# Kernel tuning notes

Measured on AMD Instinct MI355X. Metric: run time of the kernel, lower is better.

Reference implementation:

```python
import jax, jax.numpy as jnp
import numpy as np

B, T, D = 2, 2048, 2048
Q_HEADS, KV_HEADS, HEAD_DIM = 16, 4, 128
ROPE_BASE = 10000.0


def _apply_rotary(x_nhd, positions_n):
    # x_nhd: (N, H, head_dim); half-split rotary embedding.
    half = x_nhd.shape[-1] // 2
    inv_freq = 1.0 / (ROPE_BASE ** (jnp.arange(half, dtype=jnp.float32) / half))
    ang = positions_n.astype(jnp.float32)[:, None] * inv_freq  # (N, half)
    cos = jnp.cos(ang)[:, None, :]  # (N, 1, half)
    sin = jnp.sin(ang)[:, None, :]
    x1, x2 = x_nhd[..., :half], x_nhd[..., half:]
    return jnp.concatenate([x1 * cos - x2 * sin, x1 * sin + x2 * cos], axis=-1)


def setup_inputs() -> dict:
    key = jax.random.key(0)
    ks = jax.random.split(key, 5)
    s_in = 1.0 / np.sqrt(D)
    s_o = 1.0 / np.sqrt(Q_HEADS * HEAD_DIM)
    x = jax.random.normal(ks[0], (B, T, D), dtype=jnp.float32)
    positions = jnp.broadcast_to(jnp.arange(T, dtype=jnp.int32), (B, T))
    wq = jax.random.normal(ks[1], (Q_HEADS * HEAD_DIM, D), dtype=jnp.float32) * s_in
    wk = jax.random.normal(ks[2], (KV_HEADS * HEAD_DIM, D), dtype=jnp.float32) * s_in
    wv = jax.random.normal(ks[3], (KV_HEADS * HEAD_DIM, D), dtype=jnp.float32) * s_in
    wo = jax.random.normal(ks[4], (D, Q_HEADS * HEAD_DIM), dtype=jnp.float32) * s_o
    return {"x": x, "positions": positions, "wq": wq, "wk": wk, "wv": wv, "wo": wo}


def reference(x, positions, wq, wk, wv, wo):
    bsz, tsz, _ = x.shape
    q = jnp.einsum('btd,od->bto', x, wq).reshape(bsz, tsz, Q_HEADS, HEAD_DIM)
    k = jnp.einsum('btd,od->bto', x, wk).reshape(bsz, tsz, KV_HEADS, HEAD_DIM)
    v = jnp.einsum('btd,od->bto', x, wv).reshape(bsz, tsz, KV_HEADS, HEAD_DIM)
    pos_flat = positions.reshape(-1)
    q = _apply_rotary(q.reshape(-1, Q_HEADS, HEAD_DIM), pos_flat).reshape(bsz, tsz, Q_HEADS, HEAD_DIM)
    k = _apply_rotary(k.reshape(-1, KV_HEADS, HEAD_DIM), pos_flat).reshape(bsz, tsz, KV_HEADS, HEAD_DIM)
    rep = Q_HEADS // KV_HEADS
    k = jnp.repeat(k, rep, axis=2)
    v = jnp.repeat(v, rep, axis=2)
    logits = jnp.einsum('bthd,bThd->bhtT', q, k) / jnp.sqrt(jnp.float32(HEAD_DIM))
    causal = jnp.tril(jnp.ones((tsz, tsz), dtype=bool))
    logits = jnp.where(causal[None, None], logits, -1e9)
    weights = jax.nn.softmax(logits, axis=-1)
    ctx = jnp.einsum('bhtT,bThd->bthd', weights, v).reshape(bsz, tsz, Q_HEADS * HEAD_DIM)
    return jnp.einsum('bto,do->btd', ctx, wo)
```

## Files before the change

kernel.cpp:

```cpp
#include <hip/hip_runtime.h>
#include <hip/hip_bf16.h>

typedef __bf16 bf16x8 __attribute__((ext_vector_type(8)));
typedef float  f32x4  __attribute__((ext_vector_type(4)));
typedef float  f32x16 __attribute__((ext_vector_type(16)));
typedef unsigned int u32x2 __attribute__((ext_vector_type(2)));

#define B_   2
#define T_   2048
#define D_   2048
#define QH_  16
#define KVH_ 4
#define HD_  128
#define BT_  (B_ * T_)
#define KVD_ 512
#define SCL  0.12751744f

#define GLOAD_LDS16(g, l)                                        \
  __builtin_amdgcn_global_load_lds(                              \
      (const __attribute__((address_space(1))) void*)(g),        \
      (__attribute__((address_space(3))) void*)(l), 16, 0, 0)

__global__ __launch_bounds__(256) void cvt_all(
    const float* __restrict__ x, const float* __restrict__ wq,
    const float* __restrict__ wk, const float* __restrict__ wv,
    const float* __restrict__ wo, ushort* __restrict__ out) {
  const int i = blockIdx.x * 256 + threadIdx.x;
  int j = i;
  const float* src;
  float mul = 1.f;
  if (j < 2097152) { src = x; }
  else if ((j -= 2097152) < 1048576) { src = wq; mul = SCL; }
  else if ((j -= 1048576) < 262144)  { src = wk; }
  else if ((j -= 262144) < 262144)   { src = wv; }
  else { j -= 262144; src = wo; }
  float4 v = ((const float4*)src)[j];
  __hip_bfloat16 h0 = __float2bfloat16(v.x * mul);
  __hip_bfloat16 h1 = __float2bfloat16(v.y * mul);
  __hip_bfloat16 h2 = __float2bfloat16(v.z * mul);
  __hip_bfloat16 h3 = __float2bfloat16(v.w * mul);
  ushort4 o;
  o.x = *(ushort*)&h0; o.y = *(ushort*)&h1;
  o.z = *(ushort*)&h2; o.w = *(ushort*)&h3;
  ((ushort4*)out)[i] = o;
}

__global__ __launch_bounds__(256) void gemm_qkv(
    const ushort* __restrict__ X, const ushort* __restrict__ WQ,
    const ushort* __restrict__ WK, const ushort* __restrict__ WV,
    ushort* __restrict__ qo, ushort* __restrict__ ko, ushort* __restrict__ vo) {
  const int nb = blockIdx.x % 24;
  const int mb = blockIdx.x / 24;
  const int tid = threadIdx.x;
  const int wave = tid >> 6;
  const int lane = tid & 63;
  const int mrow = lane & 15;
  const int quad = lane >> 4;
  const int wm = wave >> 1;
  const int wn = wave & 1;
  const int m0 = mb * 128;
  const int K = D_;

  const ushort* Wg;
  if (nb < 16)      Wg = WQ + (size_t)nb * 128 * K;
  else if (nb < 20) Wg = WK + (size_t)(nb - 16) * 128 * K;
  else              Wg = WV + (size_t)(nb - 20) * 128 * K;

  __shared__ __align__(16) ushort At[2][128 * 64];
  __shared__ __align__(16) ushort Bt[2][128 * 64];

  f32x4 acc[4][4];
#pragma unroll
  for (int i = 0; i < 4; ++i)
#pragma unroll
    for (int j = 0; j < 4; ++j) acc[i][j] = (f32x4){0.f, 0.f, 0.f, 0.f};

  const ushort* Xg = X + (size_t)m0 * K;

  auto STAGE = [&](int buf, int k0) {
#pragma unroll
    for (int p = 0; p < 4; ++p) {
      const int c = p * 256 + tid;
      const int row = c >> 3;
      const int cc = (c & 7) ^ (row & 7);
      GLOAD_LDS16(Xg + (size_t)row * K + k0 + cc * 8,
                  At[buf] + (size_t)(p * 256 + wave * 64) * 8);
      GLOAD_LDS16(Wg + (size_t)row * K + k0 + cc * 8,
                  Bt[buf] + (size_t)(p * 256 + wave * 64) * 8);
    }
  };

  const int NT = K / 64;
  STAGE(0, 0);
  STAGE(1, 64);

  for (int t = 0; t < NT; ++t) {
    const int cur = t & 1;
    if (t + 2 < NT) asm volatile("s_waitcnt vmcnt(8)" ::: "memory");
    else            asm volatile("s_waitcnt vmcnt(0)" ::: "memory");
    __builtin_amdgcn_s_barrier();

    const ushort* Ac = At[cur];
    const ushort* Bc = Bt[cur];
#pragma unroll
    for (int s = 0; s < 2; ++s) {
      bf16x8 af[4], bfr[4];
#pragma unroll
      for (int mt = 0; mt < 4; ++mt) {
        const int row = wm * 64 + mt * 16 + mrow;
        af[mt] = *reinterpret_cast<const bf16x8*>(
            Ac + row * 64 + (((s * 4 + quad) ^ (row & 7)) * 8));
      }
#pragma unroll
      for (int nt = 0; nt < 4; ++nt) {
        const int row = wn * 64 + nt * 16 + mrow;
        bfr[nt] = *reinterpret_cast<const bf16x8*>(
            Bc + row * 64 + (((s * 4 + quad) ^ (row & 7)) * 8));
      }
#pragma unroll
      for (int mt = 0; mt < 4; ++mt)
#pragma unroll
        for (int nt = 0; nt < 4; ++nt)
          acc[mt][nt] = __builtin_amdgcn_mfma_f32_16x16x32_bf16(
              af[mt], bfr[nt], acc[mt][nt], 0, 0, 0);
    }

    asm volatile("s_waitcnt lgkmcnt(0)" ::: "memory");
    __builtin_amdgcn_s_barrier();
    if (t + 2 < NT) STAGE(cur, (t + 2) * 64);
  }

#pragma unroll
  for (int mt = 0; mt < 4; ++mt) {
#pragma unroll
    for (int nt = 0; nt < 4; ++nt) {
      const int colw = wn * 64 + nt * 16 + mrow;
      const int row0 = m0 + wm * 64 + mt * 16 + quad * 4;
      if (nb < 16) {
        const int col = nb * 128 + colw;
#pragma unroll
        for (int r = 0; r < 4; ++r) {
          __hip_bfloat16 hh = __float2bfloat16(acc[mt][nt][r]);
          qo[(size_t)(row0 + r) * 2048 + col] = *(ushort*)&hh;
        }
      } else if (nb < 20) {
        const int col = (nb - 16) * 128 + colw;
#pragma unroll
        for (int r = 0; r < 4; ++r) {
          __hip_bfloat16 hh = __float2bfloat16(acc[mt][nt][r]);
          ko[(size_t)(row0 + r) * KVD_ + col] = *(ushort*)&hh;
        }
      } else {
        const int col = (nb - 20) * 128 + colw;
        const int bb = row0 >> 11;
        const int t0 = row0 & (T_ - 1);
        ushort4 s4;
#pragma unroll
        for (int r = 0; r < 4; ++r) {
          __hip_bfloat16 hh = __float2bfloat16(acc[mt][nt][r]);
          (&s4.x)[r] = *(ushort*)&hh;
        }
        *(ushort4*)(vo + ((size_t)(bb * KVD_ + col)) * T_ + t0) = s4;
      }
    }
  }
}

__global__ __launch_bounds__(256) void gemm_o(
    const ushort* __restrict__ X, const ushort* __restrict__ W,
    float* __restrict__ Y, int M, int N, int K) {
  const int nb128 = N >> 7;
  const int mb = blockIdx.x / nb128;
  const int nb = blockIdx.x % nb128;
  const int tid = threadIdx.x;
  const int wave = tid >> 6;
  const int lane = tid & 63;
  const int mrow = lane & 15;
  const int quad = lane >> 4;
  const int wm = wave >> 1;
  const int wn = wave & 1;
  const int m0 = mb * 128;
  const int n0 = nb * 128;

  __shared__ __align__(16) ushort At[2][128 * 64];
  __shared__ __align__(16) ushort Bt[2][128 * 64];

  f32x4 acc[4][4];
#pragma unroll
  for (int i = 0; i < 4; ++i)
#pragma unroll
    for (int j = 0; j < 4; ++j) acc[i][j] = (f32x4){0.f, 0.f, 0.f, 0.f};

  const ushort* Xg = X + (size_t)m0 * K;
  const ushort* Wg = W + (size_t)n0 * K;

  auto STAGE = [&](int buf, int k0) {
#pragma unroll
    for (int p = 0; p < 4; ++p) {
      const int c = p * 256 + tid;
      const int row = c >> 3;
      const int cc = (c & 7) ^ (row & 7);
      GLOAD_LDS16(Xg + (size_t)row * K + k0 + cc * 8,
                  At[buf] + (size_t)(p * 256 + wave * 64) * 8);
      GLOAD_LDS16(Wg + (size_t)row * K + k0 + cc * 8,
                  Bt[buf] + (size_t)(p * 256 + wave * 64) * 8);
    }
  };

  const int NT = K / 64;
  STAGE(0, 0);
  STAGE(1, 64);

  for (int t = 0; t < NT; ++t) {
    const int cur = t & 1;
    if (t + 2 < NT) asm volatile("s_waitcnt vmcnt(8)" ::: "memory");
    else            asm volatile("s_waitcnt vmcnt(0)" ::: "memory");
    __builtin_amdgcn_s_barrier();

    const ushort* Ac = At[cur];
    const ushort* Bc = Bt[cur];
#pragma unroll
    for (int s = 0; s < 2; ++s) {
      bf16x8 af[4], bfr[4];
#pragma unroll
      for (int mt = 0; mt < 4; ++mt) {
        const int row = wm * 64 + mt * 16 + mrow;
        af[mt] = *reinterpret_cast<const bf16x8*>(
            Ac + row * 64 + (((s * 4 + quad) ^ (row & 7)) * 8));
      }
#pragma unroll
      for (int nt = 0; nt < 4; ++nt) {
        const int row = wn * 64 + nt * 16 + mrow;
        bfr[nt] = *reinterpret_cast<const bf16x8*>(
            Bc + row * 64 + (((s * 4 + quad) ^ (row & 7)) * 8));
      }
#pragma unroll
      for (int mt = 0; mt < 4; ++mt)
#pragma unroll
        for (int nt = 0; nt < 4; ++nt)
          acc[mt][nt] = __builtin_amdgcn_mfma_f32_16x16x32_bf16(
              af[mt], bfr[nt], acc[mt][nt], 0, 0, 0);
    }

    asm volatile("s_waitcnt lgkmcnt(0)" ::: "memory");
    __builtin_amdgcn_s_barrier();
    if (t + 2 < NT) STAGE(cur, (t + 2) * 64);
  }

#pragma unroll
  for (int mt = 0; mt < 4; ++mt)
#pragma unroll
    for (int nt = 0; nt < 4; ++nt) {
      const int col = n0 + wn * 64 + nt * 16 + mrow;
      const int row0 = m0 + wm * 64 + mt * 16 + quad * 4;
#pragma unroll
      for (int r = 0; r < 4; ++r)
        Y[(size_t)(row0 + r) * N + col] = acc[mt][nt][r];
    }
}

__global__ __launch_bounds__(256) void rope_kernel(
    __hip_bfloat16* __restrict__ q, __hip_bfloat16* __restrict__ k,
    const int* __restrict__ positions) {
  const int wave = threadIdx.x >> 6;
  const int lane = threadIdx.x & 63;
  const int p = blockIdx.x * 4 + wave;
  const int head = p % (QH_ + KVH_);
  const int bt = p / (QH_ + KVH_);

  __hip_bfloat16* base;
  if (head < QH_) base = q + ((size_t)bt * QH_ + head) * HD_;
  else            base = k + ((size_t)bt * KVH_ + (head - QH_)) * HD_;

  const float pos = (float)positions[bt];
  const float inv_freq = exp2f((float)lane * -0.20762050593f);
  const float ang = pos * inv_freq;
  const float c = cosf(ang);
  const float s = sinf(ang);

  const float x1 = __bfloat162float(base[lane]);
  const float x2 = __bfloat162float(base[lane + 64]);
  base[lane]      = __float2bfloat16(x1 * c - x2 * s);
  base[lane + 64] = __float2bfloat16(x1 * s + x2 * c);
}

static __device__ __forceinline__ unsigned pk2(float a, float b) {
  __hip_bfloat16 ha = __float2bfloat16(a);
  __hip_bfloat16 hb = __float2bfloat16(b);
  return (unsigned)(*(ushort*)&ha) | ((unsigned)(*(ushort*)&hb) << 16);
}

static __device__ __forceinline__ void hswap(unsigned& a, unsigned& b,
                                             const int hi) {
#if __has_builtin(__builtin_amdgcn_permlane32_swap)
  u32x2 r = __builtin_amdgcn_permlane32_swap(a, b, false, false);
  a = r.x;
  b = r.y;
#else
  unsigned s = __shfl_xor(hi ? a : b, 32, 64);
  unsigned na = hi ? s : a;
  b = hi ? b : s;
  a = na;
#endif
}

__global__ __launch_bounds__(256, 2) void attn_mfma(
    const ushort* __restrict__ q, const ushort* __restrict__ k,
    const ushort* __restrict__ vt, ushort* __restrict__ ctx) {
  const int tid = threadIdx.x;
  const int wave = tid >> 6;
  const int lane = tid & 63;
  const int m5 = lane & 31;
  const int hi = lane >> 5;

  int i = blockIdx.x;
  int bh, qt;
  if (i < 256) { bh = i >> 5; qt = 63 - (i & 31); }
  else { i -= 256; bh = i >> 5; qt = i & 31; }
  const int hkv = bh & 3;
  const int b   = bh >> 2;
  const int h   = hkv * 4 + wave;
  const int q0  = qt * 32;

  __shared__ __align__(16) ushort kt[2][64 * 128];
  __shared__ __align__(16) ushort vtile[2][128 * 64];

  const ushort* qrow =
      q + ((size_t)(b * T_ + q0 + m5) * QH_ + h) * HD_ + hi * 8;
  bf16x8 qf[8];
#pragma unroll
  for (int c = 0; c < 8; ++c)
    qf[c] = *reinterpret_cast<const bf16x8*>(qrow + c * 16);

  f32x16 o4[4];
#pragma unroll
  for (int dt = 0; dt < 4; ++dt)
#pragma unroll
    for (int r = 0; r < 16; ++r) o4[dt][r] = 0.f;
  float ls = 0.f;

  const ushort* kbase = k + ((size_t)b * T_ * KVH_ + hkv) * HD_;
  const ushort* vbase = vt + (size_t)(b * KVD_ + hkv * HD_) * T_;

  const int nblk = (q0 + 32 + 63) >> 6;

#pragma unroll
  for (int p = 0; p < 4; ++p) {
    const int c = p * 256 + tid;
    const int krow = c >> 4;
    const int kco = (c & 15) ^ (krow & 15);
    GLOAD_LDS16(kbase + (size_t)krow * KVD_ + kco * 8,
                kt[0] + (size_t)(p * 256 + wave * 64) * 8);
    const int vrow = c >> 3;
    const int vco = (c & 7) ^ (vrow & 7);
    GLOAD_LDS16(vbase + (size_t)vrow * T_ + vco * 8,
                vtile[0] + (size_t)(p * 256 + wave * 64) * 8);
  }
  __syncthreads();

  for (int blk = 0; blk < nblk; ++blk) {
    const int cur = blk & 1;
    const int j0 = blk * 64;

    if (blk + 1 < nblk) {
      const int j1 = j0 + 64;
#pragma unroll
      for (int p = 0; p < 4; ++p) {
        const int c = p * 256 + tid;
        const int krow = c >> 4;
        const int kco = (c & 15) ^ (krow & 15);
        GLOAD_LDS16(kbase + (size_t)(j1 + krow) * KVD_ + kco * 8,
                    kt[cur ^ 1] + (size_t)(p * 256 + wave * 64) * 8);
        const int vrow = c >> 3;
        const int vco = (c & 7) ^ (vrow & 7);
        GLOAD_LDS16(vbase + (size_t)vrow * T_ + j1 + vco * 8,
                    vtile[cur ^ 1] + (size_t)(p * 256 + wave * 64) * 8);
      }
    }

    const ushort* pk_ = kt[cur];
    const ushort* pv = vtile[cur];

#pragma unroll
    for (int t2 = 0; t2 < 2; ++t2) {
      f32x16 sa0, sa1;
#pragma unroll
      for (int r = 0; r < 16; ++r) { sa0[r] = 0.f; sa1[r] = 0.f; }
      const int rowk = t2 * 32 + m5;
#pragma unroll
      for (int c = 0; c < 8; c += 2) {
        const int ch0 = (2 * c + hi) ^ (rowk & 15);
        bf16x8 kf0 =
            *reinterpret_cast<const bf16x8*>(pk_ + rowk * 128 + ch0 * 8);
        sa0 = __builtin_amdgcn_mfma_f32_32x32x16_bf16(kf0, qf[c], sa0, 0, 0, 0);
        const int ch1 = (2 * (c + 1) + hi) ^ (rowk & 15);
        bf16x8 kf1 =
            *reinterpret_cast<const bf16x8*>(pk_ + rowk * 128 + ch1 * 8);
        sa1 = __builtin_amdgcn_mfma_f32_32x32x16_bf16(kf1, qf[c + 1], sa1,
                                                      0, 0, 0);
      }
      f32x16 sa = sa0 + sa1;

      float p[16];
      if (blk == nblk - 1) {
#pragma unroll
        for (int r = 0; r < 16; ++r) {
          const int key = j0 + t2 * 32 + (r & 3) + 8 * (r >> 2) + 4 * hi;
          p[r] = (key > q0 + m5) ? 0.f : exp2f(sa[r]);
        }
      } else {
#pragma unroll
        for (int r = 0; r < 16; ++r) p[r] = exp2f(sa[r]);
      }
#pragma unroll
      for (int r = 0; r < 16; ++r) ls += p[r];

      unsigned u0 = pk2(p[0], p[1]),   u1 = pk2(p[2], p[3]);
      unsigned u2 = pk2(p[4], p[5]),   u3 = pk2(p[6], p[7]);
      unsigned u4 = pk2(p[8], p[9]),   u5 = pk2(p[10], p[11]);
      unsigned u6 = pk2(p[12], p[13]), u7 = pk2(p[14], p[15]);
      hswap(u0, u2, hi); hswap(u1, u3, hi);
      hswap(u4, u6, hi); hswap(u5, u7, hi);

#pragma unroll
      for (int half = 0; half < 2; ++half) {
        union { unsigned w[4]; bf16x8 v; } pa;
        pa.w[0] = half ? u4 : u0;
        pa.w[1] = half ? u5 : u1;
        pa.w[2] = half ? u6 : u2;
        pa.w[3] = half ? u7 : u3;
        const int c = t2 * 2 + half;
#pragma unroll
        for (int dt = 0; dt < 4; ++dt) {
          const int rowv = dt * 32 + m5;
          const int chv = (2 * c + hi) ^ (rowv & 7);
          bf16x8 vf =
              *reinterpret_cast<const bf16x8*>(pv + rowv * 64 + chv * 8);
          o4[dt] =
              __builtin_amdgcn_mfma_f32_32x32x16_bf16(pa.v, vf, o4[dt], 0, 0, 0);
        }
      }
    }

    __syncthreads();
  }

  const float lt = ls + __shfl_xor(ls, 32, 64);
#pragma unroll
  for (int reg = 0; reg < 16; ++reg) {
    const int qrw = (reg & 3) + 8 * (reg >> 2) + 4 * hi;
    const float rl = 1.f / __shfl(lt, qrw, 64);
    ushort* op =
        ctx + ((size_t)(b * T_ + q0 + qrw) * QH_ + h) * HD_ + m5;
#pragma unroll
    for (int dt = 0; dt < 4; ++dt) {
      __hip_bfloat16 hb = __float2bfloat16(o4[dt][reg] * rl);
      op[dt * 32] = *(ushort*)&hb;
    }
  }
}

extern "C" void kernel_launch(void* const* d_in, const int* in_sizes, int n_in,
                              void* d_out, int out_size, void* d_ws, size_t ws_size,
                              hipStream_t stream) {
  const float* x  = (const float*)d_in[0];
  const int* pos  = (const int*)d_in[1];
  const float* wq = (const float*)d_in[2];
  const float* wk = (const float*)d_in[3];
  const float* wv = (const float*)d_in[4];
  const float* wo = (const float*)d_in[5];

  ushort* xb  = (ushort*)d_ws;
  ushort* wqb = xb  + (size_t)8388608;
  ushort* wkb = wqb + (size_t)4194304;
  ushort* wvb = wkb + (size_t)1048576;
  ushort* wob = wvb + (size_t)1048576;
  ushort* qb  = wob + (size_t)4194304;
  ushort* kb  = qb  + (size_t)8388608;
  ushort* vtb = kb  + (size_t)2097152;
  ushort* ctx = xb;

  cvt_all<<<18432, 256, 0, stream>>>(x, wq, wk, wv, wo, (ushort*)d_ws);

  gemm_qkv<<<(BT_ / 128) * 24, 256, 0, stream>>>(xb, wqb, wkb, wvb, qb, kb, vtb);

  rope_kernel<<<(BT_ * (QH_ + KVH_)) / 4, 256, 0, stream>>>(
      (__hip_bfloat16*)qb, (__hip_bfloat16*)kb, pos);

  attn_mfma<<<512, 256, 0, stream>>>(qb, kb, vtb, ctx);

  gemm_o<<<(BT_ / 128) * (D_ / 128), 256, 0, stream>>>(
      ctx, wob, (float*)d_out, BT_, D_, QH_ * HD_);
}
```

Baseline: 313.0 us.

## Split attention key range across wave pairs with 512-thread blocks and LDS reduction

Result: slower. 581.0 us (+85.6%).

```diff
diff --git a/kernel.cpp b/kernel.cpp
--- a/kernel.cpp
+++ b/kernel.cpp
@@ -20,6 +20,8 @@
   __builtin_amdgcn_global_load_lds(                              \
       (const __attribute__((address_space(1))) void*)(g),        \
       (__attribute__((address_space(3))) void*)(l), 16, 0, 0)
+
+#define SWZ(row) ((((row) >> 3) ^ (row)) & 15)
 
 __global__ __launch_bounds__(256) void cvt_all(
     const float* __restrict__ x, const float* __restrict__ wq,
@@ -304,7 +306,7 @@
 #endif
 }
 
-__global__ __launch_bounds__(256, 2) void attn_mfma(
+__global__ __launch_bounds__(512, 4) void attn_mfma(
     const ushort* __restrict__ q, const ushort* __restrict__ k,
     const ushort* __restrict__ vt, ushort* __restrict__ ctx) {
   const int tid = threadIdx.x;
@@ -312,6 +314,8 @@
   const int lane = tid & 63;
   const int m5 = lane & 31;
   const int hi = lane >> 5;
+  const int parity = wave & 1;
+  const int hh = wave >> 1;
 
   int i = blockIdx.x;
   int bh, qt;
@@ -319,14 +323,16 @@
   else { i -= 256; bh = i >> 5; qt = i & 31; }
   const int hkv = bh & 3;
   const int b   = bh >> 2;
-  const int h   = hkv * 4 + wave;
+  const int hq  = hkv * 4 + hh;
   const int q0  = qt * 32;
 
-  __shared__ __align__(16) ushort kt[2][64 * 128];
-  __shared__ __align__(16) ushort vtile[2][128 * 64];
+  __shared__ __align__(16) ushort smem[32768];
+  __shared__ float lbuf[4 * 32];
+  ushort* kt    = smem;
+  ushort* vtile = smem + 16384;
 
   const ushort* qrow =
-      q + ((size_t)(b * T_ + q0 + m5) * QH_ + h) * HD_ + hi * 8;
+      q + ((size_t)(b * T_ + q0 + m5) * QH_ + hq) * HD_ + hi * 8;
   bf16x8 qf[8];
 #pragma unroll
   for (int c = 0; c < 8; ++c)
@@ -342,120 +348,124 @@
   const ushort* kbase = k + ((size_t)b * T_ * KVH_ + hkv) * HD_;
   const ushort* vbase = vt + (size_t)(b * KVD_ + hkv * HD_) * T_;
 
-  const int nblk = (q0 + 32 + 63) >> 6;
-
-#pragma unroll
-  for (int p = 0; p < 4; ++p) {
-    const int c = p * 256 + tid;
-    const int krow = c >> 4;
-    const int kco = (c & 15) ^ (krow & 15);
-    GLOAD_LDS16(kbase + (size_t)krow * KVD_ + kco * 8,
-                kt[0] + (size_t)(p * 256 + wave * 64) * 8);
-    const int vrow = c >> 3;
-    const int vco = (c & 7) ^ (vrow & 7);
-    GLOAD_LDS16(vbase + (size_t)vrow * T_ + vco * 8,
-                vtile[0] + (size_t)(p * 256 + wave * 64) * 8);
+  const int nblk  = (q0 + 32 + 63) >> 6;
+  const int npair = (nblk + 1) >> 1;
+  const int koff  = parity * 64;
+
+  for (int pair = 0; pair < npair; ++pair) {
+    const int j0 = pair * 128;
+
+#pragma unroll
+    for (int p = 0; p < 4; ++p) {
+      const int c = p * 512 + tid;
+      const int row = c >> 4;
+      const int co = (c & 15) ^ SWZ(row);
+      GLOAD_LDS16(kbase + (size_t)(j0 + row) * KVD_ + co * 8,
+                  kt + (size_t)(p * 512 + wave * 64) * 8);
+      GLOAD_LDS16(vbase + (size_t)row * T_ + j0 + co * 8,
+                  vtile + (size_t)(p * 512 + wave * 64) * 8);
+    }
+    asm volatile("s_waitcnt vmcnt(0)" ::: "memory");
+    __builtin_amdgcn_s_barrier();
+
+    const int blk = pair * 2 + parity;
+    if (blk < nblk) {
+      __builtin_amdgcn_s_setprio(1);
+#pragma unroll
+      for (int t2 = 0; t2 < 2; ++t2) {
+        f32x16 sa0, sa1;
+#pragma unroll
+        for (int r = 0; r < 16; ++r) { sa0[r] = 0.f; sa1[r] = 0.f; }
+        const int rowk = koff + t2 * 32 + m5;
+#pragma unroll
+        for (int c = 0; c < 8; c += 2) {
+          const int ch0 = (2 * c + hi) ^ SWZ(rowk);
+          bf16x8 kf0 =
+              *reinterpret_cast<const bf16x8*>(kt + rowk * 128 + ch0 * 8);
+          sa0 = __builtin_amdgcn_mfma_f32_32x32x16_bf16(kf0, qf[c], sa0,
+                                                        0, 0, 0);
+          const int ch1 = (2 * (c + 1) + hi) ^ SWZ(rowk);
+          bf16x8 kf1 =
+              *reinterpret_cast<const bf16x8*>(kt + rowk * 128 + ch1 * 8);
+          sa1 = __builtin_amdgcn_mfma_f32_32x32x16_bf16(kf1, qf[c + 1], sa1,
+                                                        0, 0, 0);
+        }
+        f32x16 sa = sa0 + sa1;
+
+        float p[16];
+        if (blk == nblk - 1) {
+#pragma unroll
+          for (int r = 0; r < 16; ++r) {
+            const int key = j0 + koff + t2 * 32 + (r & 3) + 8 * (r >> 2) + 4 * hi;
+            p[r] = (key > q0 + m5) ? 0.f : exp2f(sa[r]);
+          }
+        } else {
+#pragma unroll
+          for (int r = 0; r < 16; ++r) p[r] = exp2f(sa[r]);
+        }
+#pragma unroll
+        for (int r = 0; r < 16; ++r) ls += p[r];
+
+        unsigned u0 = pk2(p[0], p[1]),   u1 = pk2(p[2], p[3]);
+        unsigned u2 = pk2(p[4], p[5]),   u3 = pk2(p[6], p[7]);
+        unsigned u4 = pk2(p[8], p[9]),   u5 = pk2(p[10], p[11]);
+        unsigned u6 = pk2(p[12], p[13]), u7 = pk2(p[14], p[15]);
+        hswap(u0, u2, hi); hswap(u1, u3, hi);
+        hswap(u4, u6, hi); hswap(u5, u7, hi);
+
+#pragma unroll
+        for (int half = 0; half < 2; ++half) {
+          union { unsigned w[4]; bf16x8 v; } pa;
+          pa.w[0] = half ? u4 : u0;
+          pa.w[1] = half ? u5 : u1;
+          pa.w[2] = half ? u6 : u2;
+          pa.w[3] = half ? u7 : u3;
+          const int gc2 = parity * 8 + t2 * 4 + half * 2;
+#pragma unroll
+          for (int dt = 0; dt < 4; ++dt) {
+            const int rowv = dt * 32 + m5;
+            const int chv = (gc2 + hi) ^ SWZ(rowv);
+            bf16x8 vf =
+                *reinterpret_cast<const bf16x8*>(vtile + rowv * 128 + chv * 8);
+            o4[dt] = __builtin_amdgcn_mfma_f32_32x32x16_bf16(pa.v, vf, o4[dt],
+                                                             0, 0, 0);
+          }
+        }
+      }
+      __builtin_amdgcn_s_setprio(0);
+    }
+
+    asm volatile("s_waitcnt lgkmcnt(0)" ::: "memory");
+    __builtin_amdgcn_s_barrier();
+  }
+
+  const float lt = ls + __shfl_xor(ls, 32, 64);
+  float* sO = (float*)smem;
+  if (parity) {
+#pragma unroll
+    for (int reg = 0; reg < 16; ++reg) {
+      const int qrw = (reg & 3) + 8 * (reg >> 2) + 4 * hi;
+#pragma unroll
+      for (int dt = 0; dt < 4; ++dt)
+        sO[hh * 4096 + qrw * 128 + dt * 32 + m5] = o4[dt][reg];
+    }
+    if (hi == 0) lbuf[hh * 32 + m5] = lt;
   }
   __syncthreads();
-
-  for (int blk = 0; blk < nblk; ++blk) {
-    const int cur = blk & 1;
-    const int j0 = blk * 64;
-
-    if (blk + 1 < nblk) {
-      const int j1 = j0 + 64;
-#pragma unroll
-      for (int p = 0; p < 4; ++p) {
-        const int c = p * 256 + tid;
-        const int krow = c >> 4;
-        const int kco = (c & 15) ^ (krow & 15);
-        GLOAD_LDS16(kbase + (size_t)(j1 + krow) * KVD_ + kco * 8,
-                    kt[cur ^ 1] + (size_t)(p * 256 + wave * 64) * 8);
-        const int vrow = c >> 3;
-        const int vco = (c & 7) ^ (vrow & 7);
-        GLOAD_LDS16(vbase + (size_t)vrow * T_ + j1 + vco * 8,
-                    vtile[cur ^ 1] + (size_t)(p * 256 + wave * 64) * 8);
-      }
-    }
-
-    const ushort* pk_ = kt[cur];
-    const ushort* pv = vtile[cur];
-
-#pragma unroll
-    for (int t2 = 0; t2 < 2; ++t2) {
-      f32x16 sa0, sa1;
-#pragma unroll
-      for (int r = 0; r < 16; ++r) { sa0[r] = 0.f; sa1[r] = 0.f; }
-      const int rowk = t2 * 32 + m5;
-#pragma unroll
-      for (int c = 0; c < 8; c += 2) {
-        const int ch0 = (2 * c + hi) ^ (rowk & 15);
-        bf16x8 kf0 =
-            *reinterpret_cast<const bf16x8*>(pk_ + rowk * 128 + ch0 * 8);
-        sa0 = __builtin_amdgcn_mfma_f32_32x32x16_bf16(kf0, qf[c], sa0, 0, 0, 0);
-        const int ch1 = (2 * (c + 1) + hi) ^ (rowk & 15);
-        bf16x8 kf1 =
-            *reinterpret_cast<const bf16x8*>(pk_ + rowk * 128 + ch1 * 8);
-        sa1 = __builtin_amdgcn_mfma_f32_32x32x16_bf16(kf1, qf[c + 1], sa1,
-                                                      0, 0, 0);
-      }
-      f32x16 sa = sa0 + sa1;
-
-      float p[16];
-      if (blk == nblk - 1) {
-#pragma unroll
-        for (int r = 0; r < 16; ++r) {
-          const int key = j0 + t2 * 32 + (r & 3) + 8 * (r >> 2) + 4 * hi;
-          p[r] = (key > q0 + m5) ? 0.f : exp2f(sa[r]);
-        }
-      } else {
-#pragma unroll
-        for (int r = 0; r < 16; ++r) p[r] = exp2f(sa[r]);
-      }
-#pragma unroll
-      for (int r = 0; r < 16; ++r) ls += p[r];
-
-      unsigned u0 = pk2(p[0], p[1]),   u1 = pk2(p[2], p[3]);
-      unsigned u2 = pk2(p[4], p[5]),   u3 = pk2(p[6], p[7]);
-      unsigned u4 = pk2(p[8], p[9]),   u5 = pk2(p[10], p[11]);
-      unsigned u6 = pk2(p[12], p[13]), u7 = pk2(p[14], p[15]);
-      hswap(u0, u2, hi); hswap(u1, u3, hi);
-      hswap(u4, u6, hi); hswap(u5, u7, hi);
-
-#pragma unroll
-      for (int half = 0; half < 2; ++half) {
-        union { unsigned w[4]; bf16x8 v; } pa;
-        pa.w[0] = half ? u4 : u0;
-        pa.w[1] = half ? u5 : u1;
-        pa.w[2] = half ? u6 : u2;
-        pa.w[3] = half ? u7 : u3;
-        const int c = t2 * 2 + half;
-#pragma unroll
-        for (int dt = 0; dt < 4; ++dt) {
-          const int rowv = dt * 32 + m5;
-          const int chv = (2 * c + hi) ^ (rowv & 7);
-          bf16x8 vf =
-              *reinterpret_cast<const bf16x8*>(pv + rowv * 64 + chv * 8);
-          o4[dt] =
-              __builtin_amdgcn_mfma_f32_32x32x16_bf16(pa.v, vf, o4[dt], 0, 0, 0);
-        }
-      }
-    }
-
-    __syncthreads();
-  }
-
-  const float lt = ls + __shfl_xor(ls, 32, 64);
-#pragma unroll
-  for (int reg = 0; reg < 16; ++reg) {
-    const int qrw = (reg & 3) + 8 * (reg >> 2) + 4 * hi;
-    const float rl = 1.f / __shfl(lt, qrw, 64);
-    ushort* op =
-        ctx + ((size_t)(b * T_ + q0 + qrw) * QH_ + h) * HD_ + m5;
-#pragma unroll
-    for (int dt = 0; dt < 4; ++dt) {
-      __hip_bfloat16 hb = __float2bfloat16(o4[dt][reg] * rl);
-      op[dt * 32] = *(ushort*)&hb;
+  if (!parity) {
+    const float ltot = lt + lbuf[hh * 32 + m5];
+#pragma unroll
+    for (int reg = 0; reg < 16; ++reg) {
+      const int qrw = (reg & 3) + 8 * (reg >> 2) + 4 * hi;
+      const float rl = 1.f / __shfl(ltot, qrw, 64);
+      ushort* op =
+          ctx + ((size_t)(b * T_ + q0 + qrw) * QH_ + hq) * HD_ + m5;
+#pragma unroll
+      for (int dt = 0; dt < 4; ++dt) {
+        const float ov = o4[dt][reg] + sO[hh * 4096 + qrw * 128 + dt * 32 + m5];
+        __hip_bfloat16 hb = __float2bfloat16(ov * rl);
+        op[dt * 32] = *(ushort*)&hb;
+      }
     }
   }
 }
@@ -487,7 +497,7 @@
   rope_kernel<<<(BT_ * (QH_ + KVH_)) / 4, 256, 0, stream>>>(
       (__hip_bfloat16*)qb, (__hip_bfloat16*)kb, pos);
 
-  attn_mfma<<<512, 256, 0, stream>>>(qb, kb, vtb, ctx);
+  attn_mfma<<<512, 512, 0, stream>>>(qb, kb, vtb, ctx);
 
   gemm_o<<<(BT_ / 128) * (D_ / 128), 256, 0, stream>>>(
       ctx, wob, (float*)d_out, BT_, D_, QH_ * HD_);
```
